# Kernel tuning notes

Measured on AMD Instinct MI355X. Metric: run time of the kernel, lower is better.

## Reference

```python
import jax, jax.numpy as jnp
from jax import lax
import numpy as np

B, P, T, K = 8, 8192, 128, 16   # events, points/event, max_tokens, k_neighbors
N = B * P
FEAT, TOK = 32, 768
NEG = jnp.finfo(jnp.float32).min


def _fps(x):
    # x: [B, P, 4] -> sel: [B, T] local FPS indices.
    # First pick = farthest from segment mean; then iteratively pick argmax of
    # min-distance-to-selected, marking chosen points with NEG (as in torch code).
    mean = x.mean(axis=1, keepdims=True)
    d2mean = jnp.sum((x - mean) ** 2, axis=-1)              # [B, P]
    bidx = jnp.arange(B)

    def update(min_d2, sel):
        c = x[bidx, sel]                                     # [B, 4]
        d2 = jnp.sum((x - c[:, None, :]) ** 2, axis=-1)      # [B, P]
        return jnp.minimum(min_d2, d2).at[bidx, sel].set(NEG)

    first = jnp.argmax(d2mean, axis=1)                       # [B]
    min_d2 = update(jnp.full((B, P), jnp.inf, x.dtype), first)

    def step(min_d2, _):
        sel = jnp.argmax(min_d2, axis=1)
        return update(min_d2, sel), sel

    _, rest = lax.scan(step, min_d2, None, length=T - 1)     # rest: [T-1, B]
    return jnp.concatenate([first[:, None], rest.T], axis=1)  # [B, T]


def _forward(coords, features, times, W0, b0, W1, b1, W2, b2, W3, b3, Wn0, bn0, Wn1, bn1):
    xyzt = jnp.concatenate([coords, times], axis=-1)         # [N, 4]
    # point-feature MLP: 32 -> 256 -> 512 -> 768 (ReLU) -> 768 (linear)
    h = jax.nn.relu(features @ W0 + b0)
    h = jax.nn.relu(h @ W1 + b1)
    h = jax.nn.relu(h @ W2 + b2)
    pf = (h @ W3 + b3).reshape(B, P, TOK)                    # [B, P, TOK]

    x = xyzt.reshape(B, P, 4)                                # equal contiguous segments
    sel = _fps(x)                                            # [B, T]
    centroids = x[jnp.arange(B)[:, None], sel]               # [B, T, 4]

    # squared distances centroid->all points in same segment (same kNN as cdist p=2)
    c2 = jnp.sum(centroids ** 2, axis=-1)                    # [B, T]
    p2 = jnp.sum(x ** 2, axis=-1)                            # [B, P]
    d2 = c2[:, :, None] + p2[:, None, :] - 2.0 * jnp.einsum('btd,bpd->btp', centroids, x)
    _, knn = lax.top_k(-d2, K)                               # [B, T, K] smallest-dist indices

    gathered = pf[jnp.arange(B)[:, None, None], knn]         # [B, T, K, TOK]
    pooled = gathered.max(axis=2)                            # [B, T, TOK]
    tokens = jax.nn.relu(pooled @ Wn0 + bn0) @ Wn1 + bn1     # neighborhood MLP
    mask = jnp.ones((B, T), dtype=bool)                      # T << P, all slots valid
    return tokens, centroids, mask


def setup_inputs() -> dict:
    key = jax.random.key(0)
    ks = jax.random.split(key, 12)

    def lin(k, i, o):
        s = 1.0 / np.sqrt(i)
        k1, k2 = jax.random.split(k)
        return (jax.random.uniform(k1, (i, o), jnp.float32, -s, s),
                jax.random.uniform(k2, (o,), jnp.float32, -s, s))

    W0, b0 = lin(ks[3], FEAT, 256)
    W1, b1 = lin(ks[4], 256, 512)
    W2, b2 = lin(ks[5], 512, 768)
    W3, b3 = lin(ks[6], 768, TOK)
    Wn0, bn0 = lin(ks[7], TOK, TOK)
    Wn1, bn1 = lin(ks[8], TOK, TOK)
    return dict(
        coords=jax.random.normal(ks[0], (N, 3), jnp.float32),
        features=jax.random.normal(ks[1], (N, FEAT), jnp.float32),
        batch_ids=jnp.arange(N, dtype=jnp.int32) // P,
        times=jax.random.normal(ks[2], (N, 1), jnp.float32),
        W0=W0, b0=b0, W1=W1, b1=b1, W2=W2, b2=b2, W3=W3, b3=b3,
        Wn0=Wn0, bn0=bn0, Wn1=Wn1, bn1=bn1,
    )


def reference(coords, features, batch_ids, times, W0, b0, W1, b1, W2, b2, W3, b3, Wn0, bn0, Wn1, bn1):
    del batch_ids  # equal contiguous segments are encoded by the [B, P] reshape
    return _forward(coords, features, times, W0, b0, W1, b1, W2, b2, W3, b3, Wn0, bn0, Wn1, bn1)
```

## Files before the change

kernel.cpp:

```cpp
#include <hip/hip_runtime.h>
#include <stdint.h>

typedef unsigned short u16;
typedef __attribute__((ext_vector_type(8))) short short8;
typedef __attribute__((ext_vector_type(4))) float f32x4;
typedef __attribute__((ext_vector_type(2))) float f32x2;

#define NEG_F (-3.402823466e+38f)

__device__ __forceinline__ u16 f2bf(float x) {
    uint32_t u = __builtin_bit_cast(uint32_t, x);
    u = (u + 0x7fffu + ((u >> 16) & 1u)) >> 16;
    return (u16)u;
}

__device__ __forceinline__ void gload_lds16(const void* g, void* l) {
    __builtin_amdgcn_global_load_lds((const __attribute__((address_space(1))) void*)g,
                                     (__attribute__((address_space(3))) void*)l, 16, 0, 0);
}

template <int CTRL, int RMASK>
__device__ __forceinline__ void argmax_dpp_step(float& v, int& i) {
    const int vb = __builtin_bit_cast(int, v);
    const int vv = __builtin_amdgcn_update_dpp(vb, vb, CTRL, RMASK, 0xf, false);
    const int ii = __builtin_amdgcn_update_dpp(i, i, CTRL, RMASK, 0xf, false);
    const float fv = __builtin_bit_cast(float, vv);
    if (fv > v || (fv == v && ii < i)) { v = fv; i = ii; }
}

__device__ __forceinline__ void argmax_wave(float& v, int& i) {
    argmax_dpp_step<0x111, 0xf>(v, i);
    argmax_dpp_step<0x112, 0xf>(v, i);
    argmax_dpp_step<0x114, 0xf>(v, i);
    argmax_dpp_step<0x118, 0xf>(v, i);
    argmax_dpp_step<0x142, 0xa>(v, i);
    argmax_dpp_step<0x143, 0xc>(v, i);
}

template <int CTRL, int RMASK>
__device__ __forceinline__ unsigned long long dppmax_u64(unsigned long long k) {
    const int lo = (int)(uint32_t)(k & 0xffffffffull);
    const int hi = (int)(uint32_t)(k >> 32);
    const int lo2 = __builtin_amdgcn_update_dpp(lo, lo, CTRL, RMASK, 0xf, false);
    const int hi2 = __builtin_amdgcn_update_dpp(hi, hi, CTRL, RMASK, 0xf, false);
    const unsigned long long o =
        ((unsigned long long)(uint32_t)hi2 << 32) | (uint32_t)lo2;
    return (o > k) ? o : k;
}
template <int CTRL, int RMASK>
__device__ __forceinline__ unsigned long long dppmin_u64(unsigned long long k) {
    const int lo = (int)(uint32_t)(k & 0xffffffffull);
    const int hi = (int)(uint32_t)(k >> 32);
    const int lo2 = __builtin_amdgcn_update_dpp(lo, lo, CTRL, RMASK, 0xf, false);
    const int hi2 = __builtin_amdgcn_update_dpp(hi, hi, CTRL, RMASK, 0xf, false);
    const unsigned long long o =
        ((unsigned long long)(uint32_t)hi2 << 32) | (uint32_t)lo2;
    return (o < k) ? o : k;
}

template <int K, int N, int KP>
__device__ __forceinline__ void tp_one(const float* __restrict__ W, u16* __restrict__ Wt, int local) {
    const int n = local / KP;
    const int k = local - n * KP;
    const float v = (k < K) ? W[(size_t)k * N + n] : 0.0f;
    Wt[local] = f2bf(v);
}

__global__ __launch_bounds__(512, 2) void fps_kernel(const float* __restrict__ coords,
                                                     const float* __restrict__ times,
                                                     float* __restrict__ cent_out,
                                                     float* __restrict__ mask_out,
                                                     const float* __restrict__ W0,
                                                     const float* __restrict__ W1,
                                                     const float* __restrict__ W2,
                                                     const float* __restrict__ W3,
                                                     const float* __restrict__ Wn0,
                                                     const float* __restrict__ Wn1,
                                                     u16* __restrict__ W0t, u16* __restrict__ W1t,
                                                     u16* __restrict__ W2t, u16* __restrict__ W3t,
                                                     u16* __restrict__ Wn0t, u16* __restrict__ Wn1t) {
    const int tid = threadIdx.x;

    if (blockIdx.x >= 8) {
        const int idx = (blockIdx.x - 8) * 512 + tid;
        if (idx < 8192) tp_one<32, 256, 32>(W0, W0t, idx);
        else if (idx < 139264) tp_one<256, 512, 256>(W1, W1t, idx - 8192);
        else if (idx < 532480) tp_one<512, 768, 512>(W2, W2t, idx - 139264);
        else if (idx < 1122304) tp_one<768, 768, 768>(W3, W3t, idx - 532480);
        else if (idx < 1712128) tp_one<768, 768, 768>(Wn0, Wn0t, idx - 1122304);
        else tp_one<768, 768, 768>(Wn1, Wn1t, idx - 1712128);
        return;
    }

    const int b = blockIdx.x;
    const int lane = tid & 63;
    const int wid = tid >> 6;

    __shared__ f32x4 pts[8192];
    __shared__ f32x4 cent_lds[128];
    __shared__ unsigned long long kslot[2][8];
    __shared__ float redv[16][4];

    f32x2 pxy[16], pzw[16];
    float md[16];
    float sx[2] = {0.f, 0.f}, sy[2] = {0.f, 0.f}, sz[2] = {0.f, 0.f}, sw[2] = {0.f, 0.f};
#pragma unroll
    for (int jj = 0; jj < 16; ++jj) {
        const int p = jj * 512 + tid;
        const int n = b * 8192 + p;
        const float x = coords[3 * n + 0];
        const float y = coords[3 * n + 1];
        const float z = coords[3 * n + 2];
        const float w = times[n];
        pxy[jj] = f32x2{x, y};
        pzw[jj] = f32x2{z, w};
        pts[p] = f32x4{x, y, z, w};
        const int q = jj & 1;
        sx[q] += x; sy[q] += y; sz[q] += z; sw[q] += w;
        md[jj] = __builtin_inff();
    }
#pragma unroll
    for (int jj = 0; jj < 16; ++jj) {
        asm volatile("" : "+v"(pxy[jj]), "+v"(pzw[jj]));
    }

#pragma unroll
    for (int q = 0; q < 2; ++q) {
        float ax = sx[q], ay = sy[q], az = sz[q], aw = sw[q];
#pragma unroll
        for (int off = 32; off > 0; off >>= 1) {
            ax += __shfl_down(ax, off);
            ay += __shfl_down(ay, off);
            az += __shfl_down(az, off);
            aw += __shfl_down(aw, off);
        }
        if (lane == 0) {
            redv[wid + 8 * q][0] = ax;
            redv[wid + 8 * q][1] = ay;
            redv[wid + 8 * q][2] = az;
            redv[wid + 8 * q][3] = aw;
        }
    }
    __syncthreads();
    float c0 = 0.f, c1 = 0.f, c2 = 0.f, c3 = 0.f;
#pragma unroll
    for (int w = 0; w < 16; ++w) { c0 += redv[w][0]; c1 += redv[w][1]; c2 += redv[w][2]; c3 += redv[w][3]; }
    c0 *= (1.0f / 8192.0f);
    c1 *= (1.0f / 8192.0f);
    c2 *= (1.0f / 8192.0f);
    c3 *= (1.0f / 8192.0f);
    f32x2 cxy = f32x2{c0, c1};
    f32x2 czw = f32x2{c2, c3};

    {
        float v = -__builtin_inff();
        int jb = 0;
#pragma unroll
        for (int jj = 0; jj < 16; ++jj) {
            const f32x2 d01 = pxy[jj] - cxy;
            const f32x2 d23 = pzw[jj] - czw;
            f32x2 s = d01 * d01;
            s += d23 * d23;
            const float d2 = s[0] + s[1];
            if (d2 > v) { v = d2; jb = jj; }
        }
        int idx = jb * 512 + tid;
        argmax_wave(v, idx);
        if (lane == 63) {
            const uint32_t bv = __builtin_bit_cast(uint32_t, v);
            const uint32_t mk = (bv & 0x80000000u) ? ~bv : (bv | 0x80000000u);
            kslot[0][wid] = ((unsigned long long)mk << 32) | (uint32_t)(0x7FFFFFFF - idx);
        }
        __syncthreads();
        unsigned long long k = kslot[0][lane & 7];
        k = dppmax_u64<0x111, 0xf>(k);
        k = dppmax_u64<0x112, 0xf>(k);
        k = dppmax_u64<0x114, 0xf>(k);
        const int klo = __builtin_amdgcn_readlane((int)(uint32_t)(k & 0xffffffffull), 7);
        const int sel = 0x7FFFFFFF - klo;
        const f32x4 C = pts[sel];
        cxy = f32x2{C[0], C[1]};
        czw = f32x2{C[2], C[3]};
        if (tid == (sel & 511)) {
            const int js = sel >> 9;
#pragma unroll
            for (int jj = 0; jj < 16; ++jj)
                if (jj == js) md[jj] = NEG_F;
        }
        if (tid == 0) cent_lds[0] = C;
    }

    for (int t = 1; t < 128; ++t) {
        float v = -__builtin_inff();
        int jb = 0;
#pragma unroll
        for (int jj = 0; jj < 16; ++jj) {
            const f32x2 d01 = pxy[jj] - cxy;
            const f32x2 d23 = pzw[jj] - czw;
            f32x2 s = d01 * d01;
            s += d23 * d23;
            const float d2 = s[0] + s[1];
            const float nm = fminf(md[jj], d2);
            md[jj] = nm;
            if (nm > v) { v = nm; jb = jj; }
        }
        int idx = jb * 512 + tid;
        argmax_wave(v, idx);
        if (lane == 63) {
            const uint32_t bv = __builtin_bit_cast(uint32_t, v);
            const uint32_t mk = (bv & 0x80000000u) ? ~bv : (bv | 0x80000000u);
            kslot[t & 1][wid] = ((unsigned long long)mk << 32) | (uint32_t)(0x7FFFFFFF - idx);
        }
        __syncthreads();
        unsigned long long k = kslot[t & 1][lane & 7];
        k = dppmax_u64<0x111, 0xf>(k);
        k = dppmax_u64<0x112, 0xf>(k);
        k = dppmax_u64<0x114, 0xf>(k);
        const int klo = __builtin_amdgcn_readlane((int)(uint32_t)(k & 0xffffffffull), 7);
        const int sel = 0x7FFFFFFF - klo;
        const f32x4 C = pts[sel];
        cxy = f32x2{C[0], C[1]};
        czw = f32x2{C[2], C[3]};
        if (tid == (sel & 511)) {
            const int js = sel >> 9;
#pragma unroll
            for (int jj = 0; jj < 16; ++jj)
                if (jj == js) md[jj] = NEG_F;
        }
        if (tid == t) cent_lds[t] = C;
    }
    if (tid < 128) {
        const f32x4 C = cent_lds[tid];
        f32x4* dst = (f32x4*)(cent_out + (size_t)(b * 128 + tid) * 4);
        *dst = C;
        mask_out[b * 128 + tid] = 1.0f;
    }
}

__global__ __launch_bounds__(256) void knn_l1_kernel(const float* __restrict__ coords,
                                                     const float* __restrict__ times,
                                                     const float* __restrict__ cent,
                                                     const float* __restrict__ feat,
                                                     const u16* __restrict__ W0t,
                                                     const float* __restrict__ b0,
                                                     u16* __restrict__ h1) {
    __shared__ unsigned long long kslot[2][4];
    __shared__ int sel_lds[16];
    __shared__ __align__(16) u16 At[16 * 32];
    __shared__ __align__(16) u16 Wt[256 * 32];
    const int q = blockIdx.x;
    const int b = q >> 7;
    const int tid = threadIdx.x;
    const int lane = tid & 63;
    const int wid = tid >> 6;

#pragma unroll
    for (int i = 0; i < 4; ++i) {
        const int e = i * 256 + tid;
        ((short8*)Wt)[e] = ((const short8*)W0t)[e];
    }

    const float c0 = cent[q * 4 + 0], c1 = cent[q * 4 + 1], c2 = cent[q * 4 + 2], c3 = cent[q * 4 + 3];
    const float cc = c0 * c0 + c1 * c1 + c2 * c2 + c3 * c3;
    float d2r[32];
#pragma unroll
    for (int s = 0; s < 32; ++s) {
        const int n = b * 8192 + s * 256 + tid;
        const float x0 = coords[3 * n], x1 = coords[3 * n + 1], x2 = coords[3 * n + 2], x3 = times[n];
        const float pp = x0 * x0 + x1 * x1 + x2 * x2 + x3 * x3;
        const float dt = x0 * c0 + x1 * c1 + x2 * c2 + x3 * c3;
        d2r[s] = cc + pp - 2.0f * dt;
    }
    for (int r = 0; r < 16; ++r) {
        float v = __builtin_inff();
        int idx = 1 << 30;
#pragma unroll
        for (int s = 0; s < 32; ++s) {
            if (d2r[s] < v) { v = d2r[s]; idx = s * 256 + tid; }
        }
        const uint32_t bv = __builtin_bit_cast(uint32_t, v);
        const uint32_t mk = (bv & 0x80000000u) ? ~bv : (bv | 0x80000000u);
        unsigned long long key = ((unsigned long long)mk << 32) | (uint32_t)idx;
        key = dppmin_u64<0x111, 0xf>(key);
        key = dppmin_u64<0x112, 0xf>(key);
        key = dppmin_u64<0x114, 0xf>(key);
        key = dppmin_u64<0x118, 0xf>(key);
        key = dppmin_u64<0x142, 0xa>(key);
        key = dppmin_u64<0x143, 0xc>(key);
        if (lane == 63) kslot[r & 1][wid] = key;
        __syncthreads();
        unsigned long long k = kslot[r & 1][lane & 3];
        k = dppmin_u64<0x111, 0xf>(k);
        k = dppmin_u64<0x112, 0xf>(k);
        const int sel = __builtin_amdgcn_readlane((int)(uint32_t)(k & 0xffffffffull), 3);
        if (tid == 0) sel_lds[r] = sel;
        if (tid == (sel & 255)) {
            const int js = sel >> 8;
#pragma unroll
            for (int s = 0; s < 32; ++s)
                if (s == js) d2r[s] = __builtin_inff();
        }
    }
    __syncthreads();
#pragma unroll
    for (int i = 0; i < 2; ++i) {
        const int e = i * 256 + tid;
        const int r = e >> 5;
        const int c = e & 31;
        const int n = b * 8192 + sel_lds[r];
        At[e] = f2bf(feat[(size_t)n * 32 + c]);
    }
    __syncthreads();
    const int arow = lane & 15;
    const int koff = (lane >> 4) * 8;
    const short8 afrag = *(const short8*)(At + arow * 32 + koff);
#pragma unroll
    for (int i = 0; i < 4; ++i) {
        const int nbase = (wid * 4 + i) * 16;
        const short8 bfrag = *(const short8*)(Wt + (nbase + (lane & 15)) * 32 + koff);
        f32x4 acc = f32x4{0.f, 0.f, 0.f, 0.f};
        acc = __builtin_amdgcn_mfma_f32_16x16x32_bf16(afrag, bfrag, acc, 0, 0, 0);
        const int col = nbase + (lane & 15);
        const float bv = b0[col];
        const int row0 = (lane >> 4) * 4;
#pragma unroll
        for (int rg = 0; rg < 4; ++rg) {
            const float vv = fmaxf(acc[rg] + bv, 0.0f);
            h1[(size_t)(q * 16 + row0 + rg) * 256 + col] = f2bf(vv);
        }
    }
}

template <int RELU, int OUTF32, int POOL>
__global__ __launch_bounds__(256) void gemm_kernel(const u16* __restrict__ A,
                                                   const u16* __restrict__ Bt,
                                                   const float* __restrict__ bias,
                                                   void* __restrict__ Cv,
                                                   int M, int N, int K) {
    (void)M;
    __shared__ __align__(16) u16 As[128 * 64];
    __shared__ __align__(16) u16 Bs[128 * 64];
    const int tid = threadIdx.x;
    const int lane = tid & 63;
    const int wid = tid >> 6;
    const int brow = blockIdx.x * 128;
    const int bcol = blockIdx.y * 128;
    const int wm = (wid >> 1) * 64;
    const int wn = (wid & 1) * 64;

    f32x4 acc[4][4];
#pragma unroll
    for (int m = 0; m < 4; ++m)
#pragma unroll
        for (int n = 0; n < 4; ++n)
            acc[m][n] = f32x4{0.f, 0.f, 0.f, 0.f};

    const int srow = tid >> 3;
    const int schunk = tid & 7;
    const uint32_t lds_wave_base = (uint32_t)(wid * 1024);

    for (int k0 = 0; k0 < K; k0 += 64) {
#pragma unroll
        for (int i = 0; i < 4; ++i) {
            const int row = i * 32 + srow;
            const int sc = schunk ^ (row & 7);
            const u16* ga = A + (size_t)(brow + row) * K + (size_t)(k0 + sc * 8);
            const u16* gb = Bt + (size_t)(bcol + row) * K + (size_t)(k0 + sc * 8);
            const uint32_t lb = (uint32_t)(i * 4096) + lds_wave_base;
            gload_lds16(ga, (char*)As + lb);
            gload_lds16(gb, (char*)Bs + lb);
        }
        __syncthreads();
#pragma unroll
        for (int kc = 0; kc < 2; ++kc) {
            short8 af[4], bfr[4];
#pragma unroll
            for (int m = 0; m < 4; ++m) {
                const int row = wm + m * 16 + (lane & 15);
                const int sc = (kc * 4 + (lane >> 4)) ^ (row & 7);
                af[m] = *(const short8*)(As + row * 64 + sc * 8);
            }
#pragma unroll
            for (int n = 0; n < 4; ++n) {
                const int row = wn + n * 16 + (lane & 15);
                const int sc = (kc * 4 + (lane >> 4)) ^ (row & 7);
                bfr[n] = *(const short8*)(Bs + row * 64 + sc * 8);
            }
#pragma unroll
            for (int m = 0; m < 4; ++m)
#pragma unroll
                for (int n = 0; n < 4; ++n)
                    acc[m][n] = __builtin_amdgcn_mfma_f32_16x16x32_bf16(af[m], bfr[n], acc[m][n], 0, 0, 0);
        }
        __syncthreads();
    }

    if (POOL) {
#pragma unroll
        for (int m = 0; m < 4; ++m) {
            const int prow = (brow >> 4) + (wm >> 4) + m;
#pragma unroll
            for (int n = 0; n < 4; ++n) {
                float v = fmaxf(fmaxf(acc[m][n][0], acc[m][n][1]),
                                fmaxf(acc[m][n][2], acc[m][n][3]));
                v = fmaxf(v, __shfl_xor(v, 16));
                v = fmaxf(v, __shfl_xor(v, 32));
                const int col = bcol + wn + n * 16 + (lane & 15);
                v += bias[col];
                if (lane < 16) ((u16*)Cv)[(size_t)prow * N + col] = f2bf(v);
            }
        }
    } else {
#pragma unroll
        for (int m = 0; m < 4; ++m) {
            const int row0 = brow + wm + m * 16 + ((lane >> 4) << 2);
#pragma unroll
            for (int n = 0; n < 4; ++n) {
                const int col = bcol + wn + n * 16 + (lane & 15);
                const float bv = bias[col];
#pragma unroll
                for (int r = 0; r < 4; ++r) {
                    float v = acc[m][n][r] + bv;
                    if (RELU) v = fmaxf(v, 0.0f);
                    if (OUTF32) ((float*)Cv)[(size_t)(row0 + r) * N + col] = v;
                    else ((u16*)Cv)[(size_t)(row0 + r) * N + col] = f2bf(v);
                }
            }
        }
    }
}

extern "C" void kernel_launch(void* const* d_in, const int* in_sizes, int n_in,
                              void* d_out, int out_size, void* d_ws, size_t ws_size,
                              hipStream_t stream) {
    (void)in_sizes; (void)n_in; (void)out_size; (void)ws_size;
    const float* coords = (const float*)d_in[0];
    const float* features = (const float*)d_in[1];
    const float* times = (const float*)d_in[3];
    const float* W0 = (const float*)d_in[4];
    const float* b0 = (const float*)d_in[5];
    const float* W1 = (const float*)d_in[6];
    const float* b1 = (const float*)d_in[7];
    const float* W2 = (const float*)d_in[8];
    const float* b2 = (const float*)d_in[9];
    const float* W3 = (const float*)d_in[10];
    const float* b3 = (const float*)d_in[11];
    const float* Wn0 = (const float*)d_in[12];
    const float* bn0 = (const float*)d_in[13];
    const float* Wn1 = (const float*)d_in[14];
    const float* bn1 = (const float*)d_in[15];

    char* ws = (char*)d_ws;
    u16* W0t = (u16*)(ws + 81920);
    u16* W1t = (u16*)(ws + 114688);
    u16* W2t = (u16*)(ws + 376832);
    u16* W3t = (u16*)(ws + 1163264);
    u16* Wn0t = (u16*)(ws + 2342912);
    u16* Wn1t = (u16*)(ws + 3522560);
    u16* bufX = (u16*)(ws + 4702208);
    u16* bufY = (u16*)(ws + 29868032);

    float* tokens_out = (float*)d_out;
    float* cent_out = (float*)d_out + 786432;
    float* mask_out = (float*)d_out + 786432 + 4096;

    fps_kernel<<<4504, 512, 0, stream>>>(coords, times, cent_out, mask_out,
                                         W0, W1, W2, W3, Wn0, Wn1,
                                         W0t, W1t, W2t, W3t, Wn0t, Wn1t);
    knn_l1_kernel<<<1024, 256, 0, stream>>>(coords, times, cent_out, features,
                                            W0t, b0, bufX);

    gemm_kernel<1, 0, 0><<<dim3(128, 4), 256, 0, stream>>>(bufX, W1t, b1, bufY, 16384, 512, 256);
    gemm_kernel<1, 0, 0><<<dim3(128, 6), 256, 0, stream>>>(bufY, W2t, b2, bufX, 16384, 768, 512);
    gemm_kernel<0, 0, 1><<<dim3(128, 6), 256, 0, stream>>>(bufX, W3t, b3, bufY, 16384, 768, 768);

    gemm_kernel<1, 0, 0><<<dim3(8, 6), 256, 0, stream>>>(bufY, Wn0t, bn0, bufX, 1024, 768, 768);
    gemm_kernel<0, 1, 0><<<dim3(8, 6), 256, 0, stream>>>(bufX, Wn1t, bn1, tokens_out, 1024, 768, 768);
}
```

Before: 291.1 us.

## Vectorize FPS distance loop as SoA packed pairs and use 64-row tiles for small GEMMs

```diff
diff --git a/kernel.cpp b/kernel.cpp
--- a/kernel.cpp
+++ b/kernel.cpp
@@ -17,6 +17,13 @@
 __device__ __forceinline__ void gload_lds16(const void* g, void* l) {
     __builtin_amdgcn_global_load_lds((const __attribute__((address_space(1))) void*)g,
                                      (__attribute__((address_space(3))) void*)l, 16, 0, 0);
+}
+
+__device__ __forceinline__ f32x2 pkmin2(f32x2 a, f32x2 b) {
+    return f32x2{fminf(a[0], b[0]), fminf(a[1], b[1])};
+}
+__device__ __forceinline__ f32x2 pkmax2(f32x2 a, f32x2 b) {
+    return f32x2{fmaxf(a[0], b[0]), fmaxf(a[1], b[1])};
 }
 
 template <int CTRL, int RMASK>
@@ -101,32 +108,37 @@
     __shared__ unsigned long long kslot[2][8];
     __shared__ float redv[16][4];
 
-    f32x2 pxy[16], pzw[16];
-    float md[16];
-    float sx[2] = {0.f, 0.f}, sy[2] = {0.f, 0.f}, sz[2] = {0.f, 0.f}, sw[2] = {0.f, 0.f};
-#pragma unroll
-    for (int jj = 0; jj < 16; ++jj) {
-        const int p = jj * 512 + tid;
-        const int n = b * 8192 + p;
-        const float x = coords[3 * n + 0];
-        const float y = coords[3 * n + 1];
-        const float z = coords[3 * n + 2];
-        const float w = times[n];
-        pxy[jj] = f32x2{x, y};
-        pzw[jj] = f32x2{z, w};
-        pts[p] = f32x4{x, y, z, w};
-        const int q = jj & 1;
-        sx[q] += x; sy[q] += y; sz[q] += z; sw[q] += w;
-        md[jj] = __builtin_inff();
-    }
-#pragma unroll
-    for (int jj = 0; jj < 16; ++jj) {
-        asm volatile("" : "+v"(pxy[jj]), "+v"(pzw[jj]));
+    f32x2 X[8], Y[8], Z[8], W_[8], md2[8];
+    f32x2 sxv = f32x2{0.f, 0.f}, syv = f32x2{0.f, 0.f};
+    f32x2 szv = f32x2{0.f, 0.f}, swv = f32x2{0.f, 0.f};
+#pragma unroll
+    for (int p = 0; p < 8; ++p) {
+        const int pa = (2 * p) * 512 + tid;
+        const int pb = (2 * p + 1) * 512 + tid;
+        const int na = b * 8192 + pa;
+        const int nb = b * 8192 + pb;
+        const float xa = coords[3 * na + 0], ya = coords[3 * na + 1], za = coords[3 * na + 2], wa = times[na];
+        const float xb = coords[3 * nb + 0], yb = coords[3 * nb + 1], zb = coords[3 * nb + 2], wb = times[nb];
+        pts[pa] = f32x4{xa, ya, za, wa};
+        pts[pb] = f32x4{xb, yb, zb, wb};
+        X[p] = f32x2{xa, xb};
+        Y[p] = f32x2{ya, yb};
+        Z[p] = f32x2{za, zb};
+        W_[p] = f32x2{wa, wb};
+        sxv += X[p]; syv += Y[p]; szv += Z[p]; swv += W_[p];
+        md2[p] = f32x2{__builtin_inff(), __builtin_inff()};
+    }
+#pragma unroll
+    for (int p = 0; p < 8; ++p) {
+        asm volatile("" : "+v"(X[p]), "+v"(Y[p]), "+v"(Z[p]), "+v"(W_[p]));
     }
 
 #pragma unroll
     for (int q = 0; q < 2; ++q) {
-        float ax = sx[q], ay = sy[q], az = sz[q], aw = sw[q];
+        float ax = (q == 0) ? sxv[0] : sxv[1];
+        float ay = (q == 0) ? syv[0] : syv[1];
+        float az = (q == 0) ? szv[0] : szv[1];
+        float aw = (q == 0) ? swv[0] : swv[1];
 #pragma unroll
         for (int off = 32; off > 0; off >>= 1) {
             ax += __shfl_down(ax, off);
@@ -149,20 +161,31 @@
     c1 *= (1.0f / 8192.0f);
     c2 *= (1.0f / 8192.0f);
     c3 *= (1.0f / 8192.0f);
-    f32x2 cxy = f32x2{c0, c1};
-    f32x2 czw = f32x2{c2, c3};
+    f32x2 cX = f32x2{c0, c0}, cY = f32x2{c1, c1}, cZ = f32x2{c2, c2}, cW = f32x2{c3, c3};
 
     {
-        float v = -__builtin_inff();
+        f32x2 vp = f32x2{-__builtin_inff(), -__builtin_inff()};
+        f32x2 t2[8];
+#pragma unroll
+        for (int p = 0; p < 8; ++p) {
+            const f32x2 dX = X[p] - cX;
+            const f32x2 dY = Y[p] - cY;
+            const f32x2 dZ = Z[p] - cZ;
+            const f32x2 dW = W_[p] - cW;
+            f32x2 sA = dX * dX;
+            sA += dZ * dZ;
+            f32x2 sB = dY * dY;
+            sB += dW * dW;
+            const f32x2 d2p = sA + sB;
+            t2[p] = d2p;
+            vp = pkmax2(vp, d2p);
+        }
+        float v = fmaxf(vp[0], vp[1]);
         int jb = 0;
 #pragma unroll
-        for (int jj = 0; jj < 16; ++jj) {
-            const f32x2 d01 = pxy[jj] - cxy;
-            const f32x2 d23 = pzw[jj] - czw;
-            f32x2 s = d01 * d01;
-            s += d23 * d23;
-            const float d2 = s[0] + s[1];
-            if (d2 > v) { v = d2; jb = jj; }
+        for (int p = 7; p >= 0; --p) {
+            if (t2[p][1] == v) jb = 2 * p + 1;
+            if (t2[p][0] == v) jb = 2 * p;
         }
         int idx = jb * 512 + tid;
         argmax_wave(v, idx);
@@ -179,30 +202,42 @@
         const int klo = __builtin_amdgcn_readlane((int)(uint32_t)(k & 0xffffffffull), 7);
         const int sel = 0x7FFFFFFF - klo;
         const f32x4 C = pts[sel];
-        cxy = f32x2{C[0], C[1]};
-        czw = f32x2{C[2], C[3]};
+        cX = f32x2{C[0], C[0]}; cY = f32x2{C[1], C[1]};
+        cZ = f32x2{C[2], C[2]}; cW = f32x2{C[3], C[3]};
         if (tid == (sel & 511)) {
             const int js = sel >> 9;
 #pragma unroll
-            for (int jj = 0; jj < 16; ++jj)
-                if (jj == js) md[jj] = NEG_F;
+            for (int p = 0; p < 8; ++p) {
+                if (2 * p == js) md2[p][0] = NEG_F;
+                if (2 * p + 1 == js) md2[p][1] = NEG_F;
+            }
         }
         if (tid == 0) cent_lds[0] = C;
     }
 
     for (int t = 1; t < 128; ++t) {
-        float v = -__builtin_inff();
+        f32x2 vp = f32x2{-__builtin_inff(), -__builtin_inff()};
+#pragma unroll
+        for (int p = 0; p < 8; ++p) {
+            const f32x2 dX = X[p] - cX;
+            const f32x2 dY = Y[p] - cY;
+            const f32x2 dZ = Z[p] - cZ;
+            const f32x2 dW = W_[p] - cW;
+            f32x2 sA = dX * dX;
+            sA += dZ * dZ;
+            f32x2 sB = dY * dY;
+            sB += dW * dW;
+            const f32x2 d2p = sA + sB;
+            const f32x2 nmp = pkmin2(md2[p], d2p);
+            md2[p] = nmp;
+            vp = pkmax2(vp, nmp);
+        }
+        float v = fmaxf(vp[0], vp[1]);
         int jb = 0;
 #pragma unroll
-        for (int jj = 0; jj < 16; ++jj) {
-            const f32x2 d01 = pxy[jj] - cxy;
-            const f32x2 d23 = pzw[jj] - czw;
-            f32x2 s = d01 * d01;
-            s += d23 * d23;
-            const float d2 = s[0] + s[1];
-            const float nm = fminf(md[jj], d2);
-            md[jj] = nm;
-            if (nm > v) { v = nm; jb = jj; }
+        for (int p = 7; p >= 0; --p) {
+            if (md2[p][1] == v) jb = 2 * p + 1;
+            if (md2[p][0] == v) jb = 2 * p;
         }
         int idx = jb * 512 + tid;
         argmax_wave(v, idx);
@@ -219,13 +254,15 @@
         const int klo = __builtin_amdgcn_readlane((int)(uint32_t)(k & 0xffffffffull), 7);
         const int sel = 0x7FFFFFFF - klo;
         const f32x4 C = pts[sel];
-        cxy = f32x2{C[0], C[1]};
-        czw = f32x2{C[2], C[3]};
+        cX = f32x2{C[0], C[0]}; cY = f32x2{C[1], C[1]};
+        cZ = f32x2{C[2], C[2]}; cW = f32x2{C[3], C[3]};
         if (tid == (sel & 511)) {
             const int js = sel >> 9;
 #pragma unroll
-            for (int jj = 0; jj < 16; ++jj)
-                if (jj == js) md[jj] = NEG_F;
+            for (int p = 0; p < 8; ++p) {
+                if (2 * p == js) md2[p][0] = NEG_F;
+                if (2 * p + 1 == js) md2[p][1] = NEG_F;
+            }
         }
         if (tid == t) cent_lds[t] = C;
     }
@@ -331,28 +368,29 @@
     }
 }
 
-template <int RELU, int OUTF32, int POOL>
+template <int BM, int RELU, int OUTF32, int POOL>
 __global__ __launch_bounds__(256) void gemm_kernel(const u16* __restrict__ A,
                                                    const u16* __restrict__ Bt,
                                                    const float* __restrict__ bias,
                                                    void* __restrict__ Cv,
                                                    int M, int N, int K) {
     (void)M;
-    __shared__ __align__(16) u16 As[128 * 64];
+    constexpr int NREP = (BM == 128) ? 4 : 2;
+    __shared__ __align__(16) u16 As[BM * 64];
     __shared__ __align__(16) u16 Bs[128 * 64];
     const int tid = threadIdx.x;
     const int lane = tid & 63;
     const int wid = tid >> 6;
-    const int brow = blockIdx.x * 128;
+    const int brow = blockIdx.x * BM;
     const int bcol = blockIdx.y * 128;
-    const int wm = (wid >> 1) * 64;
-    const int wn = (wid & 1) * 64;
-
-    f32x4 acc[4][4];
+    const int wm = (BM == 128) ? (wid >> 1) * 64 : 0;
+    const int wn = (BM == 128) ? (wid & 1) * 64 : wid * 32;
+
+    f32x4 acc[4][NREP];
 #pragma unroll
     for (int m = 0; m < 4; ++m)
 #pragma unroll
-        for (int n = 0; n < 4; ++n)
+        for (int n = 0; n < NREP; ++n)
             acc[m][n] = f32x4{0.f, 0.f, 0.f, 0.f};
 
     const int srow = tid >> 3;
@@ -361,19 +399,25 @@
 
     for (int k0 = 0; k0 < K; k0 += 64) {
 #pragma unroll
+        for (int i = 0; i < BM / 32; ++i) {
+            const int row = i * 32 + srow;
+            const int sc = schunk ^ (row & 7);
+            const u16* ga = A + (size_t)(brow + row) * K + (size_t)(k0 + sc * 8);
+            const uint32_t lb = (uint32_t)(i * 4096) + lds_wave_base;
+            gload_lds16(ga, (char*)As + lb);
+        }
+#pragma unroll
         for (int i = 0; i < 4; ++i) {
             const int row = i * 32 + srow;
             const int sc = schunk ^ (row & 7);
-            const u16* ga = A + (size_t)(brow + row) * K + (size_t)(k0 + sc * 8);
             const u16* gb = Bt + (size_t)(bcol + row) * K + (size_t)(k0 + sc * 8);
             const uint32_t lb = (uint32_t)(i * 4096) + lds_wave_base;
-            gload_lds16(ga, (char*)As + lb);
             gload_lds16(gb, (char*)Bs + lb);
         }
         __syncthreads();
 #pragma unroll
         for (int kc = 0; kc < 2; ++kc) {
-            short8 af[4], bfr[4];
+            short8 af[4], bfr[NREP];
 #pragma unroll
             for (int m = 0; m < 4; ++m) {
                 const int row = wm + m * 16 + (lane & 15);
@@ -381,7 +425,7 @@
                 af[m] = *(const short8*)(As + row * 64 + sc * 8);
             }
 #pragma unroll
-            for (int n = 0; n < 4; ++n) {
+            for (int n = 0; n < NREP; ++n) {
                 const int row = wn + n * 16 + (lane & 15);
                 const int sc = (kc * 4 + (lane >> 4)) ^ (row & 7);
                 bfr[n] = *(const short8*)(Bs + row * 64 + sc * 8);
@@ -389,7 +433,7 @@
 #pragma unroll
             for (int m = 0; m < 4; ++m)
 #pragma unroll
-                for (int n = 0; n < 4; ++n)
+                for (int n = 0; n < NREP; ++n)
                     acc[m][n] = __builtin_amdgcn_mfma_f32_16x16x32_bf16(af[m], bfr[n], acc[m][n], 0, 0, 0);
         }
         __syncthreads();
@@ -400,7 +444,7 @@
         for (int m = 0; m < 4; ++m) {
             const int prow = (brow >> 4) + (wm >> 4) + m;
 #pragma unroll
-            for (int n = 0; n < 4; ++n) {
+            for (int n = 0; n < NREP; ++n) {
                 float v = fmaxf(fmaxf(acc[m][n][0], acc[m][n][1]),
                                 fmaxf(acc[m][n][2], acc[m][n][3]));
                 v = fmaxf(v, __shfl_xor(v, 16));
@@ -415,7 +459,7 @@
         for (int m = 0; m < 4; ++m) {
             const int row0 = brow + wm + m * 16 + ((lane >> 4) << 2);
 #pragma unroll
-            for (int n = 0; n < 4; ++n) {
+            for (int n = 0; n < NREP; ++n) {
                 const int col = bcol + wn + n * 16 + (lane & 15);
                 const float bv = bias[col];
 #pragma unroll
@@ -470,10 +514,10 @@
     knn_l1_kernel<<<1024, 256, 0, stream>>>(coords, times, cent_out, features,
                                             W0t, b0, bufX);
 
-    gemm_kernel<1, 0, 0><<<dim3(128, 4), 256, 0, stream>>>(bufX, W1t, b1, bufY, 16384, 512, 256);
-    gemm_kernel<1, 0, 0><<<dim3(128, 6), 256, 0, stream>>>(bufY, W2t, b2, bufX, 16384, 768, 512);
-    gemm_kernel<0, 0, 1><<<dim3(128, 6), 256, 0, stream>>>(bufX, W3t, b3, bufY, 16384, 768, 768);
-
-    gemm_kernel<1, 0, 0><<<dim3(8, 6), 256, 0, stream>>>(bufY, Wn0t, bn0, bufX, 1024, 768, 768);
-    gemm_kernel<0, 1, 0><<<dim3(8, 6), 256, 0, stream>>>(bufX, Wn1t, bn1, tokens_out, 1024, 768, 768);
-}
+    gemm_kernel<128, 1, 0, 0><<<dim3(128, 4), 256, 0, stream>>>(bufX, W1t, b1, bufY, 16384, 512, 256);
+    gemm_kernel<128, 1, 0, 0><<<dim3(128, 6), 256, 0, stream>>>(bufY, W2t, b2, bufX, 16384, 768, 512);
+    gemm_kernel<128, 0, 0, 1><<<dim3(128, 6), 256, 0, stream>>>(bufX, W3t, b3, bufY, 16384, 768, 768);
+
+    gemm_kernel<64, 1, 0, 0><<<dim3(16, 6), 256, 0, stream>>>(bufY, Wn0t, bn0, bufX, 1024, 768, 768);
+    gemm_kernel<64, 0, 1, 0><<<dim3(16, 6), 256, 0, stream>>>(bufX, Wn1t, bn1, tokens_out, 1024, 768, 768);
+}
```

New measurement: 284.3 us (median of 2 runs). -2.3%, faster.
